# Performance work log

Measured on AMD Instinct MI355X. Metric: run time of the kernel, lower is better.

The kernel has to match this reference:

```python
import jax, jax.numpy as jnp
import numpy as np

N = 100000      # nodes
E = 1600000     # edges (avg degree 16)
IN = 128        # in_channels
HID = 128       # hidden_channels
OUT = 2         # out_channels
NEG_SLOPE = 0.2  # PyG GATConv default


def setup_inputs() -> dict:
    key = jax.random.key(0)
    ks = jax.random.split(key, 20)
    inp = {
        "x": jax.random.normal(ks[0], (N, IN), dtype=jnp.float32),
        "edge_index": jax.random.randint(ks[1], (2, E), 0, N, dtype=jnp.int32),
    }
    # GATConv params (heads=1): W:[din,dout], attention vecs a_src/a_dst:[dout], bias:[dout]
    dims = [(IN, HID), (HID, HID), (HID, HID)]
    for i, (din, dout) in enumerate(dims, start=1):
        base = 4 * i
        inp[f"W{i}"] = jax.random.normal(ks[base], (din, dout), dtype=jnp.float32) * (1.0 / np.sqrt(din))
        inp[f"a{i}s"] = jax.random.normal(ks[base + 1], (dout,), dtype=jnp.float32) * 0.1
        inp[f"a{i}d"] = jax.random.normal(ks[base + 2], (dout,), dtype=jnp.float32) * 0.1
        inp[f"b{i}"] = jnp.zeros((dout,), dtype=jnp.float32)
    inp["Wc"] = jax.random.normal(ks[16], (HID, OUT), dtype=jnp.float32) * (1.0 / np.sqrt(HID))
    inp["bc"] = jnp.zeros((OUT,), dtype=jnp.float32)
    return inp


def _gat_layer(x, src, dst, W, a_s, a_d, b, n):
    # Linear transform: [n, dout]
    h = x @ W
    # Edge attention logits: alpha_src[j] + alpha_dst[i], LeakyReLU (PyG GATConv)
    e = jax.nn.leaky_relu(jnp.take(h @ a_s, src) + jnp.take(h @ a_d, dst), NEG_SLOPE)
    # Stable softmax over incoming edges per destination node
    m = jax.ops.segment_max(e, dst, num_segments=n)
    ex = jnp.exp(e - m[dst])
    denom = jax.ops.segment_sum(ex, dst, num_segments=n)
    alpha = ex / denom[dst]
    # Weighted scatter-aggregation of source features into destinations
    out = jax.ops.segment_sum(alpha[:, None] * jnp.take(h, src, axis=0), dst, num_segments=n)
    return out + b


def reference(x, edge_index, W1, a1s, a1d, b1, W2, a2s, a2d, b2, W3, a3s, a3d, b3, Wc, bc):
    n = x.shape[0]
    # PyG GATConv default add_self_loops=True
    loop = jnp.arange(n, dtype=edge_index.dtype)
    src = jnp.concatenate([edge_index[0], loop])
    dst = jnp.concatenate([edge_index[1], loop])
    for (W, a_s, a_d, b) in ((W1, a1s, a1d, b1), (W2, a2s, a2d, b2), (W3, a3s, a3d, b3)):
        x = jax.nn.relu(_gat_layer(x, src, dst, W, a_s, a_d, b, n))
    return x @ Wc + bc
```

## Files before the change

### kernel.cpp

```cpp
#include <hip/hip_runtime.h>
#include <hip/hip_fp16.h>

#define NNODES 100000
#define NEDGES 1600000
#define DIM 128
#define NB ((NNODES + 63) / 64)
#define NCH 128
#define CHUNK ((NEDGES + NCH - 1) / NCH)
#define EBUF 2560
#define LSTR 136

typedef _Float16 f16x8 __attribute__((ext_vector_type(8)));
typedef float f32x4 __attribute__((ext_vector_type(4)));

__device__ __forceinline__ float leaky02(float t) { return t > 0.f ? t : 0.2f * t; }

union H8u { uint2 u; __half2 h[2]; };

template <bool XF16>
__global__ __launch_bounds__(256) void gemm_mfma(const float* __restrict__ X,
                                                 const __half* __restrict__ X16,
                                                 const float* __restrict__ W,
                                                 const float* __restrict__ as_,
                                                 const float* __restrict__ ad_,
                                                 __half* __restrict__ H,
                                                 float* __restrict__ s,
                                                 float* __restrict__ d, int n) {
    __shared__ __half As[64][LSTR];
    __shared__ __half Wt[128][LSTR];
    int t = threadIdx.x;
    int brow = blockIdx.x * 64;

    if (XF16) {
        for (int i = t; i < 64 * 16; i += 256) {
            int r = i >> 4, c8 = (i & 15) * 8;
            int gr = brow + r;
            uint4 v = (gr < n) ? *(const uint4*)(X16 + (size_t)gr * 128 + c8)
                               : make_uint4(0u, 0u, 0u, 0u);
            *(uint4*)&As[r][c8] = v;
        }
    } else {
        for (int i = t; i < 64 * 32; i += 256) {
            int r = i >> 5, c4 = (i & 31) * 4;
            int gr = brow + r;
            float4 v = (gr < n) ? *(const float4*)(X + (size_t)gr * 128 + c4)
                                : make_float4(0.f, 0.f, 0.f, 0.f);
            As[r][c4 + 0] = __float2half_rn(v.x);
            As[r][c4 + 1] = __float2half_rn(v.y);
            As[r][c4 + 2] = __float2half_rn(v.z);
            As[r][c4 + 3] = __float2half_rn(v.w);
        }
    }
    for (int i = t; i < 128 * 32; i += 256) {
        int k = i >> 5, n4 = (i & 31) * 4;
        float4 wv = *(const float4*)(W + k * 128 + n4);
        Wt[n4 + 0][k] = __float2half_rn(wv.x);
        Wt[n4 + 1][k] = __float2half_rn(wv.y);
        Wt[n4 + 2][k] = __float2half_rn(wv.z);
        Wt[n4 + 3][k] = __float2half_rn(wv.w);
    }
    __syncthreads();

    int wid  = t >> 6;
    int lane = t & 63;
    int lrow = lane & 15;
    int lkg  = lane >> 4;
    int r0   = wid * 16;

    f32x4 acc[8] = {};
#pragma unroll
    for (int kk = 0; kk < 128; kk += 32) {
        f16x8 af = *(const f16x8*)&As[r0 + lrow][kk + lkg * 8];
#pragma unroll
        for (int ct = 0; ct < 8; ++ct) {
            f16x8 bf = *(const f16x8*)&Wt[ct * 16 + lrow][kk + lkg * 8];
            acc[ct] = __builtin_amdgcn_mfma_f32_16x16x32_f16(af, bf, acc[ct], 0, 0, 0);
        }
    }

    float sp[4] = {0.f, 0.f, 0.f, 0.f};
    float dp[4] = {0.f, 0.f, 0.f, 0.f};
#pragma unroll
    for (int ct = 0; ct < 8; ++ct) {
        float a_s = as_[ct * 16 + lrow];
        float a_d = ad_[ct * 16 + lrow];
#pragma unroll
        for (int j = 0; j < 4; ++j) {
            sp[j] += acc[ct][j] * a_s;
            dp[j] += acc[ct][j] * a_d;
        }
    }
#pragma unroll
    for (int j = 0; j < 4; ++j) {
        int gr = brow + r0 + lkg * 4 + j;
        if (gr < n) {
#pragma unroll
            for (int ct = 0; ct < 8; ++ct)
                H[(size_t)gr * 128 + ct * 16 + lrow] = __float2half_rn(acc[ct][j]);
        }
    }
#pragma unroll
    for (int off = 1; off < 16; off <<= 1)
#pragma unroll
        for (int j = 0; j < 4; ++j) {
            sp[j] += __shfl_xor(sp[j], off);
            dp[j] += __shfl_xor(dp[j], off);
        }
    if (lrow == 0)
#pragma unroll
        for (int j = 0; j < 4; ++j) {
            int gr = brow + r0 + lkg * 4 + j;
            if (gr < n) { s[gr] = sp[j]; d[gr] = dp[j]; }
        }
}

__global__ __launch_bounds__(512) void bucket_count(const int* __restrict__ dst,
                                                    int* __restrict__ blockcounts) {
    __shared__ int hist[NB];
    int b = blockIdx.x, t = threadIdx.x;
    for (int i = t; i < NB; i += 512) hist[i] = 0;
    __syncthreads();
    int e0 = b * CHUNK, e1 = min(NEDGES, e0 + CHUNK);
    for (int e = e0 + t; e < e1; e += 512)
        atomicAdd(&hist[dst[e] >> 6], 1);
    __syncthreads();
    for (int i = t; i < NB; i += 512)
        blockcounts[i * NCH + b] = hist[i];
}

__global__ __launch_bounds__(NCH) void bucket_scan_a(int* __restrict__ blockcounts,
                                                     int* __restrict__ btotal) {
    int bin = blockIdx.x, t = threadIdx.x;
    int v = blockcounts[bin * NCH + t];
    int incl = v;
#pragma unroll
    for (int off = 1; off < 64; off <<= 1) {
        int u = __shfl_up(incl, off, 64);
        if ((t & 63) >= off) incl += u;
    }
    __shared__ int wsum;
    if (t == 63) wsum = incl;
    __syncthreads();
    int excl = incl - v + ((t >= 64) ? wsum : 0);
    blockcounts[bin * NCH + t] = excl;
    if (t == NCH - 1) btotal[bin] = excl + v;
}

__global__ __launch_bounds__(1024) void bucket_scan_b(const int* __restrict__ btotal,
                                                      int* __restrict__ bbase) {
    __shared__ int ts[2][1024];
    int t = threadIdx.x;
    int b0 = t * 2;
    int c0 = (b0 < NB)     ? btotal[b0]     : 0;
    int c1 = (b0 + 1 < NB) ? btotal[b0 + 1] : 0;
    int sum = c0 + c1;
    ts[0][t] = sum;
    __syncthreads();
    int sb = 0;
    for (int off = 1; off < 1024; off <<= 1) {
        int v = ts[sb][t] + ((t >= off) ? ts[sb][t - off] : 0);
        ts[sb ^ 1][t] = v;
        sb ^= 1;
        __syncthreads();
    }
    int excl = ts[sb][t] - sum;
    if (b0 < NB)     bbase[b0]     = excl;
    if (b0 + 1 < NB) bbase[b0 + 1] = excl + c0;
    if (t == 1023) bbase[NB] = ts[sb][1023];
}

__global__ __launch_bounds__(512) void bucket_scatter(const int* __restrict__ src,
                                                      const int* __restrict__ dst,
                                                      const int* __restrict__ blockcounts,
                                                      const int* __restrict__ bbase,
                                                      int* __restrict__ packed) {
    __shared__ int cur[NB];
    int b = blockIdx.x, t = threadIdx.x;
    for (int i = t; i < NB; i += 512) cur[i] = bbase[i] + blockcounts[i * NCH + b];
    __syncthreads();
    int e0 = b * CHUNK, e1 = min(NEDGES, e0 + CHUNK);
    for (int e = e0 + t; e < e1; e += 512) {
        int dv = dst[e];
        int bin = dv >> 6;
        int p = atomicAdd(&cur[bin], 1);
        packed[p] = ((dv & 63) << 17) | src[e];
    }
}

__global__ __launch_bounds__(256) void bucket_csr(const int* __restrict__ packed,
                                                  const int* __restrict__ bbase,
                                                  int* __restrict__ rowptr,
                                                  int* __restrict__ csr_src) {
    __shared__ int ebuf[EBUF];
    __shared__ int hist[64], cur[64];
    int i = blockIdx.x, t = threadIdx.x;
    int base = bbase[i], cnt = bbase[i + 1] - base;
    bool inl = (cnt <= EBUF);
    if (inl) for (int j = t; j < cnt; j += 256) ebuf[j] = packed[base + j];
    if (t < 64) hist[t] = 0;
    __syncthreads();
    for (int j = t; j < cnt; j += 256) {
        int v = inl ? ebuf[j] : packed[base + j];
        atomicAdd(&hist[v >> 17], 1);
    }
    __syncthreads();
    if (t < 64) {
        int h = hist[t];
        int incl = h;
#pragma unroll
        for (int off = 1; off < 64; off <<= 1) {
            int u = __shfl_up(incl, off, 64);
            if (t >= off) incl += u;
        }
        int ex = incl - h;
        cur[t] = ex;
        int node = i * 64 + t;
        if (node <= NNODES) rowptr[node] = base + ex;
    }
    __syncthreads();
    for (int j = t; j < cnt; j += 256) {
        int v = inl ? ebuf[j] : packed[base + j];
        int off = atomicAdd(&cur[v >> 17], 1);
        csr_src[base + off] = v & 0x1FFFF;
    }
}

template <bool LAST>
__global__ __launch_bounds__(256) void gat_gather(const int* __restrict__ rowptr,
                                                  const int* __restrict__ csr,
                                                  const float* __restrict__ s,
                                                  const float* __restrict__ d,
                                                  const __half* __restrict__ H,
                                                  const float* __restrict__ bias,
                                                  const float* __restrict__ Wc,
                                                  const float* __restrict__ bc,
                                                  __half* __restrict__ A16,
                                                  float* __restrict__ out, int n) {
    int node = blockIdx.x * 4 + (threadIdx.x >> 6);
    if (node >= n) return;
    int lane = threadIdx.x & 63;
    int half = lane >> 5;
    int pos  = lane & 31;
    int base = rowptr[node];
    int deg  = rowptr[node + 1] - base;
    float dnode = d[node];
    float snode = s[node];

    float4 acc = make_float4(0.f, 0.f, 0.f, 0.f);
    float denom;

    if (deg < 64) {
        int cnt = deg + 1;
        int si  = (lane < deg) ? csr[base + lane] : node;
        float sv = (lane < deg) ? s[si] : snode;
        float lv = leaky02(sv + dnode);
        float lm = (lane < cnt) ? lv : -1e30f;
#pragma unroll
        for (int off = 32; off; off >>= 1) lm = fmaxf(lm, __shfl_xor(lm, off));
        float w = (lane < cnt) ? expf(lv - lm) : 0.f;
        denom = w;
#pragma unroll
        for (int off = 32; off; off >>= 1) denom += __shfl_xor(denom, off);

        int jfull = cnt & ~15;
        for (int j = 0; j < jfull; j += 16) {
            float wk[8]; int sk[8];
#pragma unroll
            for (int k = 0; k < 8; ++k) {
                int ii = j + 2 * k + half;
                wk[k] = __shfl(w, ii);
                sk[k] = __shfl(si, ii);
            }
            H8u hv[8];
#pragma unroll
            for (int k = 0; k < 8; ++k)
                hv[k].u = *(const uint2*)(H + (size_t)sk[k] * 128 + pos * 4);
#pragma unroll
            for (int k = 0; k < 8; ++k) {
                float2 a01 = __half22float2(hv[k].h[0]);
                float2 a23 = __half22float2(hv[k].h[1]);
                acc.x += wk[k] * a01.x;
                acc.y += wk[k] * a01.y;
                acc.z += wk[k] * a23.x;
                acc.w += wk[k] * a23.y;
            }
        }
        int rem = cnt - jfull;
        int kmax = (rem + 1) >> 1;
        for (int k = 0; k < kmax; ++k) {
            int ii = jfull + 2 * k + half;
            float wv = __shfl(w, ii);
            int   sv2 = __shfl(si, ii);
            H8u hv;
            hv.u = *(const uint2*)(H + (size_t)sv2 * 128 + pos * 4);
            float2 a01 = __half22float2(hv.h[0]);
            float2 a23 = __half22float2(hv.h[1]);
            acc.x += wv * a01.x;
            acc.y += wv * a01.y;
            acc.z += wv * a23.x;
            acc.w += wv * a23.y;
        }
    } else {
        float m = -1e30f;
        for (int c = 0; c <= deg; c += 64) {
            int idx = c + lane;
            float lv = -1e30f;
            if (idx < deg)       lv = leaky02(s[csr[base + idx]] + dnode);
            else if (idx == deg) lv = leaky02(snode + dnode);
            m = fmaxf(m, lv);
        }
#pragma unroll
        for (int off = 32; off; off >>= 1) m = fmaxf(m, __shfl_xor(m, off));
        denom = 0.f;
        for (int c = 0; c <= deg; c += 64) {
            int idx = c + lane;
            int cnt = min(64, deg + 1 - c);
            int si = (idx < deg) ? csr[base + idx] : node;
            float w = 0.f;
            if (idx < deg)       w = expf(leaky02(s[si] + dnode) - m);
            else if (idx == deg) w = expf(leaky02(snode + dnode) - m);
            denom += w;
            int cnt16 = (cnt + 15) & ~15;
            for (int j = 0; j < cnt16; j += 16) {
                float wk[8]; int sk[8];
#pragma unroll
                for (int k = 0; k < 8; ++k) {
                    int ii = j + 2 * k + half;
                    wk[k] = __shfl(w, ii);
                    sk[k] = __shfl(si, ii);
                }
                H8u hv[8];
#pragma unroll
                for (int k = 0; k < 8; ++k)
                    hv[k].u = *(const uint2*)(H + (size_t)sk[k] * 128 + pos * 4);
#pragma unroll
                for (int k = 0; k < 8; ++k) {
                    float2 a01 = __half22float2(hv[k].h[0]);
                    float2 a23 = __half22float2(hv[k].h[1]);
                    acc.x += wk[k] * a01.x;
                    acc.y += wk[k] * a01.y;
                    acc.z += wk[k] * a23.x;
                    acc.w += wk[k] * a23.y;
                }
            }
        }
#pragma unroll
        for (int off = 32; off; off >>= 1) denom += __shfl_xor(denom, off);
    }

    acc.x += __shfl_xor(acc.x, 32);
    acc.y += __shfl_xor(acc.y, 32);
    acc.z += __shfl_xor(acc.z, 32);
    acc.w += __shfl_xor(acc.w, 32);
    if (half == 0) {
        float inv = 1.f / denom;
        float4 o;
        o.x = fmaxf(acc.x * inv + bias[pos * 4 + 0], 0.f);
        o.y = fmaxf(acc.y * inv + bias[pos * 4 + 1], 0.f);
        o.z = fmaxf(acc.z * inv + bias[pos * 4 + 2], 0.f);
        o.w = fmaxf(acc.w * inv + bias[pos * 4 + 3], 0.f);
        if (!LAST) {
            H8u pk;
            pk.h[0] = __floats2half2_rn(o.x, o.y);
            pk.h[1] = __floats2half2_rn(o.z, o.w);
            *(uint2*)(A16 + (size_t)node * 128 + pos * 4) = pk.u;
        } else {
            float c0v = o.x * Wc[(pos * 4 + 0) * 2] + o.y * Wc[(pos * 4 + 1) * 2] +
                        o.z * Wc[(pos * 4 + 2) * 2] + o.w * Wc[(pos * 4 + 3) * 2];
            float c1v = o.x * Wc[(pos * 4 + 0) * 2 + 1] + o.y * Wc[(pos * 4 + 1) * 2 + 1] +
                        o.z * Wc[(pos * 4 + 2) * 2 + 1] + o.w * Wc[(pos * 4 + 3) * 2 + 1];
#pragma unroll
            for (int off = 16; off; off >>= 1) {
                c0v += __shfl_xor(c0v, off);
                c1v += __shfl_xor(c1v, off);
            }
            if (pos == 0) {
                out[(size_t)node * 2 + 0] = c0v + bc[0];
                out[(size_t)node * 2 + 1] = c1v + bc[1];
            }
        }
    }
}

extern "C" void kernel_launch(void* const* d_in, const int* in_sizes, int n_in,
                              void* d_out, int out_size, void* d_ws, size_t ws_size,
                              hipStream_t stream) {
    const float* x   = (const float*)d_in[0];
    const int*   ei  = (const int*)d_in[1];
    const int*   src = ei;
    const int*   dst = ei + NEDGES;
    const float* Ws[3]  = {(const float*)d_in[2], (const float*)d_in[6], (const float*)d_in[10]};
    const float* ass[3] = {(const float*)d_in[3], (const float*)d_in[7], (const float*)d_in[11]};
    const float* ads[3] = {(const float*)d_in[4], (const float*)d_in[8], (const float*)d_in[12]};
    const float* bs[3]  = {(const float*)d_in[5], (const float*)d_in[9], (const float*)d_in[13]};
    const float* Wc = (const float*)d_in[14];
    const float* bc = (const float*)d_in[15];
    float* out = (float*)d_out;

    const int n = NNODES;

    __half* h16  = (__half*)d_ws;
    __half* a16  = h16 + (size_t)n * DIM;
    float*  sbuf = (float*)(a16 + (size_t)n * DIM);
    float*  dbuf = sbuf + n;
    int*    rowptr      = (int*)(dbuf + n);
    int*    csr_src     = rowptr + n + 1;
    int*    packed      = csr_src + NEDGES;
    int*    blockcounts = packed + NEDGES;
    int*    bbase       = blockcounts + NB * NCH;
    int*    btotal      = bbase + NB + 1;

    const int g64         = (n + 63) / 64;
    const int gather_grid = (n + 3) / 4;

    bucket_count<<<NCH, 512, 0, stream>>>(dst, blockcounts);
    bucket_scan_a<<<NB, NCH, 0, stream>>>(blockcounts, btotal);
    bucket_scan_b<<<1, 1024, 0, stream>>>(btotal, bbase);
    bucket_scatter<<<NCH, 512, 0, stream>>>(src, dst, blockcounts, bbase, packed);
    bucket_csr<<<NB, 256, 0, stream>>>(packed, bbase, rowptr, csr_src);

    for (int layer = 0; layer < 3; ++layer) {
        if (layer == 0)
            gemm_mfma<false><<<g64, 256, 0, stream>>>(x, a16, Ws[0], ass[0], ads[0],
                                                      h16, sbuf, dbuf, n);
        else
            gemm_mfma<true><<<g64, 256, 0, stream>>>(x, a16, Ws[layer], ass[layer], ads[layer],
                                                     h16, sbuf, dbuf, n);
        if (layer == 2)
            gat_gather<true><<<gather_grid, 256, 0, stream>>>(
                rowptr, csr_src, sbuf, dbuf, h16, bs[layer], Wc, bc, a16, out, n);
        else
            gat_gather<false><<<gather_grid, 256, 0, stream>>>(
                rowptr, csr_src, sbuf, dbuf, h16, bs[layer], Wc, bc, a16, out, n);
    }
}
```

Measured before the change: 423.7 us.

## Split GAT gather into alpha and column-sliced aggregation kernels with packed edge weights

Features are stored in eight 16-column slices so each aggregation block works on one slice, which shrinks the working set of gathered rows per pass and should improve cache hit rates. Attention weights are computed once in a separate kernel and quantized to 15 bits packed with the 17-bit source index. The aggregation kernel then reads only the packed edge word per edge. The final classifier becomes its own kernel. This adds extra kernel launches and eight passes over the edge list, and the 15-bit weight quantization costs some precision.

Result: slower. 894.5 us (+111.1%).

```diff
diff --git a/kernel.cpp b/kernel.cpp
--- a/kernel.cpp
+++ b/kernel.cpp
@@ -9,6 +9,7 @@
 #define CHUNK ((NEDGES + NCH - 1) / NCH)
 #define EBUF 2560
 #define LSTR 136
+#define NSL16 ((size_t)NNODES * 16)
 
 typedef _Float16 f16x8 __attribute__((ext_vector_type(8)));
 typedef float f32x4 __attribute__((ext_vector_type(4)));
@@ -16,6 +17,7 @@
 __device__ __forceinline__ float leaky02(float t) { return t > 0.f ? t : 0.2f * t; }
 
 union H8u { uint2 u; __half2 h[2]; };
+
 
 template <bool XF16>
 __global__ __launch_bounds__(256) void gemm_mfma(const float* __restrict__ X,
@@ -35,7 +37,8 @@
         for (int i = t; i < 64 * 16; i += 256) {
             int r = i >> 4, c8 = (i & 15) * 8;
             int gr = brow + r;
-            uint4 v = (gr < n) ? *(const uint4*)(X16 + (size_t)gr * 128 + c8)
+            int sl = c8 >> 4, off = c8 & 15;
+            uint4 v = (gr < n) ? *(const uint4*)(X16 + (size_t)sl * NSL16 + (size_t)gr * 16 + off)
                                : make_uint4(0u, 0u, 0u, 0u);
             *(uint4*)&As[r][c8] = v;
         }
@@ -96,7 +99,7 @@
         if (gr < n) {
 #pragma unroll
             for (int ct = 0; ct < 8; ++ct)
-                H[(size_t)gr * 128 + ct * 16 + lrow] = __float2half_rn(acc[ct][j]);
+                H[(size_t)ct * NSL16 + (size_t)gr * 16 + lrow] = __float2half_rn(acc[ct][j]);
         }
     }
 #pragma unroll
@@ -225,29 +228,18 @@
     }
 }
 
-template <bool LAST>
-__global__ __launch_bounds__(256) void gat_gather(const int* __restrict__ rowptr,
-                                                  const int* __restrict__ csr,
-                                                  const float* __restrict__ s,
-                                                  const float* __restrict__ d,
-                                                  const __half* __restrict__ H,
-                                                  const float* __restrict__ bias,
-                                                  const float* __restrict__ Wc,
-                                                  const float* __restrict__ bc,
-                                                  __half* __restrict__ A16,
-                                                  float* __restrict__ out, int n) {
+__global__ __launch_bounds__(256) void gat_alpha(const int* __restrict__ rowptr,
+                                                 const int* __restrict__ csr,
+                                                 const float* __restrict__ s,
+                                                 const float* __restrict__ d,
+                                                 unsigned* __restrict__ packed2,
+                                                 unsigned* __restrict__ selfpk, int n) {
     int node = blockIdx.x * 4 + (threadIdx.x >> 6);
     if (node >= n) return;
     int lane = threadIdx.x & 63;
-    int half = lane >> 5;
-    int pos  = lane & 31;
     int base = rowptr[node];
     int deg  = rowptr[node + 1] - base;
-    float dnode = d[node];
-    float snode = s[node];
-
-    float4 acc = make_float4(0.f, 0.f, 0.f, 0.f);
-    float denom;
+    float dnode = d[node], snode = s[node];
 
     if (deg < 64) {
         int cnt = deg + 1;
@@ -258,48 +250,13 @@
 #pragma unroll
         for (int off = 32; off; off >>= 1) lm = fmaxf(lm, __shfl_xor(lm, off));
         float w = (lane < cnt) ? expf(lv - lm) : 0.f;
-        denom = w;
+        float denom = w;
 #pragma unroll
         for (int off = 32; off; off >>= 1) denom += __shfl_xor(denom, off);
-
-        int jfull = cnt & ~15;
-        for (int j = 0; j < jfull; j += 16) {
-            float wk[8]; int sk[8];
-#pragma unroll
-            for (int k = 0; k < 8; ++k) {
-                int ii = j + 2 * k + half;
-                wk[k] = __shfl(w, ii);
-                sk[k] = __shfl(si, ii);
-            }
-            H8u hv[8];
-#pragma unroll
-            for (int k = 0; k < 8; ++k)
-                hv[k].u = *(const uint2*)(H + (size_t)sk[k] * 128 + pos * 4);
-#pragma unroll
-            for (int k = 0; k < 8; ++k) {
-                float2 a01 = __half22float2(hv[k].h[0]);
-                float2 a23 = __half22float2(hv[k].h[1]);
-                acc.x += wk[k] * a01.x;
-                acc.y += wk[k] * a01.y;
-                acc.z += wk[k] * a23.x;
-                acc.w += wk[k] * a23.y;
-            }
-        }
-        int rem = cnt - jfull;
-        int kmax = (rem + 1) >> 1;
-        for (int k = 0; k < kmax; ++k) {
-            int ii = jfull + 2 * k + half;
-            float wv = __shfl(w, ii);
-            int   sv2 = __shfl(si, ii);
-            H8u hv;
-            hv.u = *(const uint2*)(H + (size_t)sv2 * 128 + pos * 4);
-            float2 a01 = __half22float2(hv.h[0]);
-            float2 a23 = __half22float2(hv.h[1]);
-            acc.x += wv * a01.x;
-            acc.y += wv * a01.y;
-            acc.z += wv * a23.x;
-            acc.w += wv * a23.y;
-        }
+        unsigned q = (unsigned)__float2int_rn(w / denom * 32767.f);
+        unsigned pk = ((unsigned)si << 15) | q;
+        if (lane < deg)        packed2[base + lane] = pk;
+        else if (lane == deg)  selfpk[node] = pk;
     } else {
         float m = -1e30f;
         for (int c = 0; c <= deg; c += 64) {
@@ -311,74 +268,112 @@
         }
 #pragma unroll
         for (int off = 32; off; off >>= 1) m = fmaxf(m, __shfl_xor(m, off));
-        denom = 0.f;
+        float denom = 0.f;
         for (int c = 0; c <= deg; c += 64) {
             int idx = c + lane;
-            int cnt = min(64, deg + 1 - c);
-            int si = (idx < deg) ? csr[base + idx] : node;
-            float w = 0.f;
-            if (idx < deg)       w = expf(leaky02(s[si] + dnode) - m);
-            else if (idx == deg) w = expf(leaky02(snode + dnode) - m);
-            denom += w;
-            int cnt16 = (cnt + 15) & ~15;
-            for (int j = 0; j < cnt16; j += 16) {
-                float wk[8]; int sk[8];
-#pragma unroll
-                for (int k = 0; k < 8; ++k) {
-                    int ii = j + 2 * k + half;
-                    wk[k] = __shfl(w, ii);
-                    sk[k] = __shfl(si, ii);
-                }
-                H8u hv[8];
-#pragma unroll
-                for (int k = 0; k < 8; ++k)
-                    hv[k].u = *(const uint2*)(H + (size_t)sk[k] * 128 + pos * 4);
-#pragma unroll
-                for (int k = 0; k < 8; ++k) {
-                    float2 a01 = __half22float2(hv[k].h[0]);
-                    float2 a23 = __half22float2(hv[k].h[1]);
-                    acc.x += wk[k] * a01.x;
-                    acc.y += wk[k] * a01.y;
-                    acc.z += wk[k] * a23.x;
-                    acc.w += wk[k] * a23.y;
-                }
+            if (idx < deg)       denom += expf(leaky02(s[csr[base + idx]] + dnode) - m);
+            else if (idx == deg) denom += expf(leaky02(snode + dnode) - m);
+        }
+#pragma unroll
+        for (int off = 32; off; off >>= 1) denom += __shfl_xor(denom, off);
+        for (int c = 0; c <= deg; c += 64) {
+            int idx = c + lane;
+            if (idx < deg) {
+                int si = csr[base + idx];
+                float w = expf(leaky02(s[si] + dnode) - m);
+                packed2[base + idx] = ((unsigned)si << 15) |
+                                      (unsigned)__float2int_rn(w / denom * 32767.f);
+            } else if (idx == deg) {
+                float w = expf(leaky02(snode + dnode) - m);
+                selfpk[node] = ((unsigned)node << 15) |
+                               (unsigned)__float2int_rn(w / denom * 32767.f);
             }
         }
-#pragma unroll
-        for (int off = 32; off; off >>= 1) denom += __shfl_xor(denom, off);
-    }
-
-    acc.x += __shfl_xor(acc.x, 32);
-    acc.y += __shfl_xor(acc.y, 32);
-    acc.z += __shfl_xor(acc.z, 32);
-    acc.w += __shfl_xor(acc.w, 32);
-    if (half == 0) {
-        float inv = 1.f / denom;
-        float4 o;
-        o.x = fmaxf(acc.x * inv + bias[pos * 4 + 0], 0.f);
-        o.y = fmaxf(acc.y * inv + bias[pos * 4 + 1], 0.f);
-        o.z = fmaxf(acc.z * inv + bias[pos * 4 + 2], 0.f);
-        o.w = fmaxf(acc.w * inv + bias[pos * 4 + 3], 0.f);
-        if (!LAST) {
-            H8u pk;
-            pk.h[0] = __floats2half2_rn(o.x, o.y);
-            pk.h[1] = __floats2half2_rn(o.z, o.w);
-            *(uint2*)(A16 + (size_t)node * 128 + pos * 4) = pk.u;
-        } else {
-            float c0v = o.x * Wc[(pos * 4 + 0) * 2] + o.y * Wc[(pos * 4 + 1) * 2] +
-                        o.z * Wc[(pos * 4 + 2) * 2] + o.w * Wc[(pos * 4 + 3) * 2];
-            float c1v = o.x * Wc[(pos * 4 + 0) * 2 + 1] + o.y * Wc[(pos * 4 + 1) * 2 + 1] +
-                        o.z * Wc[(pos * 4 + 2) * 2 + 1] + o.w * Wc[(pos * 4 + 3) * 2 + 1];
-#pragma unroll
-            for (int off = 16; off; off >>= 1) {
-                c0v += __shfl_xor(c0v, off);
-                c1v += __shfl_xor(c1v, off);
-            }
-            if (pos == 0) {
-                out[(size_t)node * 2 + 0] = c0v + bc[0];
-                out[(size_t)node * 2 + 1] = c1v + bc[1];
-            }
-        }
+    }
+}
+
+__global__ __launch_bounds__(256) void gat_agg(const int* __restrict__ rowptr,
+                                               const unsigned* __restrict__ packed2,
+                                               const unsigned* __restrict__ selfpk,
+                                               const __half* __restrict__ H,
+                                               const float* __restrict__ bias,
+                                               __half* __restrict__ A16, int n) {
+    int sl  = blockIdx.x & 7;
+    int ng  = blockIdx.x >> 3;
+    int wid = threadIdx.x >> 6;
+    int lane = threadIdx.x & 63;
+    int es = lane >> 2;
+    int cp = lane & 3;
+    const __half* Hs = H + (size_t)sl * NSL16;
+    __half* As = A16 + (size_t)sl * NSL16;
+    float b0 = bias[sl * 16 + cp * 4 + 0];
+    float b1 = bias[sl * 16 + cp * 4 + 1];
+    float b2 = bias[sl * 16 + cp * 4 + 2];
+    float b3 = bias[sl * 16 + cp * 4 + 3];
+
+    int node0 = (ng * 4 + wid) * 8;
+    int nend  = min(node0 + 8, n);
+    for (int node = node0; node < nend; ++node) {
+        int base = rowptr[node];
+        int deg  = rowptr[node + 1] - base;
+        f32x4 acc = {0.f, 0.f, 0.f, 0.f};
+        for (int c = 0; c <= deg; c += 16) {
+            int e = c + es;
+            unsigned pk = 0u;
+            if (e < deg)        pk = __builtin_nontemporal_load(&packed2[base + e]);
+            else if (e == deg)  pk = selfpk[node];
+            float a = (float)(pk & 0x7fffu) * (1.f / 32767.f);
+            unsigned srcv = pk >> 15;
+            H8u hv;
+            hv.u = *(const uint2*)(Hs + (size_t)srcv * 16 + cp * 4);
+            float2 a01 = __half22float2(hv.h[0]);
+            float2 a23 = __half22float2(hv.h[1]);
+            acc[0] += a * a01.x;
+            acc[1] += a * a01.y;
+            acc[2] += a * a23.x;
+            acc[3] += a * a23.y;
+        }
+#pragma unroll
+        for (int off = 4; off < 64; off <<= 1) {
+            acc[0] += __shfl_xor(acc[0], off);
+            acc[1] += __shfl_xor(acc[1], off);
+            acc[2] += __shfl_xor(acc[2], off);
+            acc[3] += __shfl_xor(acc[3], off);
+        }
+        if (es == 0) {
+            float o0 = fmaxf(acc[0] + b0, 0.f);
+            float o1 = fmaxf(acc[1] + b1, 0.f);
+            float o2 = fmaxf(acc[2] + b2, 0.f);
+            float o3 = fmaxf(acc[3] + b3, 0.f);
+            H8u pk16;
+            pk16.h[0] = __floats2half2_rn(o0, o1);
+            pk16.h[1] = __floats2half2_rn(o2, o3);
+            *(uint2*)(As + (size_t)node * 16 + cp * 4) = pk16.u;
+        }
+    }
+}
+
+__global__ __launch_bounds__(256) void classify16(const __half* __restrict__ A,
+                                                  const float* __restrict__ Wc,
+                                                  const float* __restrict__ bc,
+                                                  float* __restrict__ out, int n) {
+    int node = blockIdx.x * 4 + (threadIdx.x >> 6);
+    if (node >= n) return;
+    int lane = threadIdx.x & 63;
+    int col = lane * 2;
+    int sl = col >> 4, off = col & 15;
+    __half2 h2 = *(const __half2*)(A + (size_t)sl * NSL16 + (size_t)node * 16 + off);
+    float2 f = __half22float2(h2);
+    float o0 = f.x * Wc[col * 2]       + f.y * Wc[(col + 1) * 2];
+    float o1 = f.x * Wc[col * 2 + 1]   + f.y * Wc[(col + 1) * 2 + 1];
+#pragma unroll
+    for (int offx = 32; offx; offx >>= 1) {
+        o0 += __shfl_xor(o0, offx);
+        o1 += __shfl_xor(o1, offx);
+    }
+    if (lane == 0) {
+        out[(size_t)node * 2 + 0] = o0 + bc[0];
+        out[(size_t)node * 2 + 1] = o1 + bc[1];
     }
 }
 
@@ -399,19 +394,22 @@
 
     const int n = NNODES;
 
-    __half* h16  = (__half*)d_ws;
-    __half* a16  = h16 + (size_t)n * DIM;
-    float*  sbuf = (float*)(a16 + (size_t)n * DIM);
-    float*  dbuf = sbuf + n;
-    int*    rowptr      = (int*)(dbuf + n);
-    int*    csr_src     = rowptr + n + 1;
-    int*    packed      = csr_src + NEDGES;
-    int*    blockcounts = packed + NEDGES;
-    int*    bbase       = blockcounts + NB * NCH;
-    int*    btotal      = bbase + NB + 1;
-
-    const int g64         = (n + 63) / 64;
-    const int gather_grid = (n + 3) / 4;
+    __half*   h16  = (__half*)d_ws;
+    __half*   a16  = h16 + (size_t)n * DIM;
+    float*    sbuf = (float*)(a16 + (size_t)n * DIM);
+    float*    dbuf = sbuf + n;
+    unsigned* selfpk = (unsigned*)(dbuf + n);
+    int*      rowptr      = (int*)(selfpk + n);
+    int*      csr_src     = rowptr + n + 1;
+    int*      packed      = csr_src + NEDGES;
+    int*      blockcounts = packed + NEDGES;
+    int*      bbase       = blockcounts + NB * NCH;
+    int*      btotal      = bbase + NB + 1;
+    unsigned* packed2     = (unsigned*)packed;
+
+    const int g64       = (n + 63) / 64;
+    const int node_grid = (n + 3) / 4;
+    const int agg_grid  = ((n + 31) / 32) * 8;
 
     bucket_count<<<NCH, 512, 0, stream>>>(dst, blockcounts);
     bucket_scan_a<<<NB, NCH, 0, stream>>>(blockcounts, btotal);
@@ -426,11 +424,10 @@
         else
             gemm_mfma<true><<<g64, 256, 0, stream>>>(x, a16, Ws[layer], ass[layer], ads[layer],
                                                      h16, sbuf, dbuf, n);
-        if (layer == 2)
-            gat_gather<true><<<gather_grid, 256, 0, stream>>>(
-                rowptr, csr_src, sbuf, dbuf, h16, bs[layer], Wc, bc, a16, out, n);
-        else
-            gat_gather<false><<<gather_grid, 256, 0, stream>>>(
-                rowptr, csr_src, sbuf, dbuf, h16, bs[layer], Wc, bc, a16, out, n);
-    }
-}
+        gat_alpha<<<node_grid, 256, 0, stream>>>(rowptr, csr_src, sbuf, dbuf,
+                                                 packed2, selfpk, n);
+        gat_agg<<<agg_grid, 256, 0, stream>>>(rowptr, packed2, selfpk, h16,
+                                              bs[layer], a16, n);
+    }
+    classify16<<<node_grid, 256, 0, stream>>>(a16, Wc, bc, out, n);
+}
```
